# Kernel optimization log

Hardware: AMD Instinct MI355X
Metric: run time of the kernel (lower is better)

## Reference

```python
import jax, jax.numpy as jnp
import numpy as np

B, CIN, COUT, H, W, KH, KW, G = 16, 64, 128, 128, 128, 3, 3, 4


def setup_inputs() -> dict:
    key = jax.random.key(0)
    k1, k2, k3 = jax.random.split(key, 3)
    x = jax.random.normal(k1, (B, CIN, H, W), dtype=jnp.float32)
    spline_weights = jax.random.normal(k2, (COUT, CIN, KH, KW, G), dtype=jnp.float32)
    basis_weights = jax.random.normal(k3, (COUT, CIN, KH, KW), dtype=jnp.float32)
    return {"x": x, "spline_weights": spline_weights, "basis_weights": basis_weights}


def _conv_same(inp, w):
    # NCHW x OIHW -> NCHW, stride 1, SAME padding (pad = k//2, matches torch F.pad)
    return jax.lax.conv_general_dilated(
        inp, w, window_strides=(1, 1),
        padding=[(KH // 2, KH // 2), (KW // 2, KW // 2)],
        dimension_numbers=("NCHW", "OIHW", "NCHW"))


def reference(x, spline_weights, basis_weights):
    # spline branch: patch broadcast over grid then summed == conv with grid-summed kernel
    w_spline = spline_weights.sum(axis=-1)  # (COUT, CIN, KH, KW)
    # basis branch: silu applied to (zero-)padded patches; silu(0)=0 so equals conv(silu(x))
    return _conv_same(x, w_spline) + _conv_same(jax.nn.silu(x), basis_weights)
```

## Files before the change

kernel.cpp:

```cpp
#include <hip/hip_runtime.h>
#include <math.h>

#define B_    16
#define CIN   64
#define COUT  128
#define H_    128
#define W_    128
#define CI2   128
#define KTOT  1152

typedef __bf16 bf16x8 __attribute__((ext_vector_type(8)));
typedef float  f32x4  __attribute__((ext_vector_type(4)));

#define XT_BYTES  ((size_t)B_ * H_ * W_ * CI2 * 2)
#define WC_BYTES  ((size_t)COUT * KTOT * 2)
#define Z_OFF     (XT_BYTES + WC_BYTES)
#define WS_NEED   (Z_OFF + 4096)

__global__ __launch_bounds__(256) void w_prep(const float* __restrict__ sw,
                                              const float* __restrict__ bw,
                                              __bf16* __restrict__ wc,
                                              float* __restrict__ zp) {
    const int i = blockIdx.x * 256 + threadIdx.x;
    if (blockIdx.x == 0) zp[threadIdx.x] = 0.f;
    if (i >= COUT * KTOT) return;
    const int co = i / KTOT, k = i - co * KTOT;
    const int tap = k >> 7, ci2 = k & 127;
    float v;
    if (ci2 < CIN) {
        const float* p = sw + ((size_t)(co * CIN + ci2) * 9 + tap) * 4;
        v = p[0] + p[1] + p[2] + p[3];
    } else {
        v = bw[(size_t)(co * CIN + (ci2 - CIN)) * 9 + tap];
    }
    const int f = co >> 4, l15 = co & 15;
    const int kk = ci2 >> 6, j = (ci2 >> 5) & 1;
    const int lq = (ci2 >> 3) & 3, e = ci2 & 7;
    const int c = kk * 9 + tap;
    const size_t off = ((size_t)(c * 16 + f * 2 + j)) * 512 + (lq * 16 + l15) * 8 + e;
    wc[off] = (__bf16)v;
}

__global__ __launch_bounds__(256) void xt_prep(const float* __restrict__ x,
                                               __bf16* __restrict__ xt) {
    __shared__ __align__(16) __bf16 tile[64][136];
    const int t  = threadIdx.x;
    const int w0 = blockIdx.x * 64;
    const int h  = blockIdx.y;
    const int b  = blockIdx.z;
    const float* xb = x + ((size_t)(b * CIN) * H_ + h) * W_ + w0;
#pragma unroll
    for (int rep = 0; rep < 16; ++rep) {
        const int idx = rep * 256 + t;
        const int ci = idx >> 6, w = idx & 63;
        const float v = xb[(size_t)ci * H_ * W_ + w];
        tile[w][ci]       = (__bf16)v;
        tile[w][CIN + ci] = (__bf16)(v / (1.f + __expf(-v)));
    }
    __syncthreads();
    __bf16* ob = xt + (((size_t)b * H_ + h) * W_ + w0) * CI2;
#pragma unroll
    for (int rep = 0; rep < 4; ++rep) {
        const int idx = rep * 256 + t;
        const int w = idx >> 4, sl = idx & 15;
        *(bf16x8*)(ob + (size_t)w * CI2 + sl * 8) = *(const bf16x8*)(&tile[w][sl * 8]);
    }
}

__global__ __launch_bounds__(256, 2) void kan_mfma(const __bf16* __restrict__ xt,
                                                   const __bf16* __restrict__ wc,
                                                   const float* __restrict__ zp,
                                                   float* __restrict__ out) {
    __shared__ __align__(16) char bh[2720 * 16];
    __shared__ __align__(16) char asA[1024 * 16];
    __shared__ __align__(16) char asB[1024 * 16];
    const int t    = threadIdx.x;
    const int lane = t & 63, wn = t >> 6;
    const int l15 = lane & 15, lq = lane >> 4;

    const int orig = blockIdx.x;
    const int wid  = (orig & 7) * 128 + (orig >> 3);
    const int b  = wid >> 6;
    const int hy = (wid >> 2) & 15, wx = wid & 3;
    const int w0 = wx * 32, h0 = hy * 8;

    const size_t xbase = (size_t)b * (H_ * W_ * CI2);

#define STAGEB_(kk)                                                             \
    _Pragma("unroll")                                                           \
    for (int i = 0; i < 11; ++i) {                                              \
        const int s = i * 256 + t;                                              \
        if (s < 2720) {                                                         \
            const int cell = s >> 3, q = s & 7;                                 \
            const int ih = cell / 34, iw = cell - ih * 34;                      \
            const int gh = h0 + ih - 1, gw = w0 + iw - 1;                       \
            const int chunk = q ^ (cell & 7);                                   \
            const void* src;                                                    \
            if (gh >= 0 && gh < H_ && gw >= 0 && gw < W_)                       \
                src = (const void*)(xt + xbase +                                \
                      ((size_t)(gh * W_ + gw)) * CI2 + (kk) * 64 + chunk * 8);  \
            else                                                                \
                src = (const void*)zp;                                          \
            __builtin_amdgcn_global_load_lds(                                   \
                (const __attribute__((address_space(1))) unsigned int*)src,     \
                (__attribute__((address_space(3))) unsigned int*)(bh + s * 16), \
                16, 0, 0);                                                      \
        }                                                                       \
    }

#define STAGEC_(buf, c)                                                         \
    _Pragma("unroll")                                                           \
    for (int i = 0; i < 4; ++i) {                                               \
        const int s = i * 256 + t;                                              \
        __builtin_amdgcn_global_load_lds(                                       \
            (const __attribute__((address_space(1))) unsigned int*)              \
                (wc + (size_t)(c) * 8192 + s * 8),                              \
            (__attribute__((address_space(3))) unsigned int*)((buf) + s * 16),  \
            16, 0, 0);                                                          \
    }

#define COMPUTE_(buf, tp)                                                       \
    {                                                                           \
        const int kh_ = ((tp) * 11) >> 5;                                       \
        const int kw_ = (tp) - kh_ * 3;                                         \
        _Pragma("unroll")                                                       \
        for (int j = 0; j < 2; ++j) {                                           \
            bf16x8 af[8], bf[4];                                                \
            _Pragma("unroll")                                                   \
            for (int m = 0; m < 8; ++m)                                         \
                af[m] = *(const bf16x8*)((buf) + (m * 2 + j) * 1024 +           \
                                         lane * 16);                            \
            _Pragma("unroll")                                                   \
            for (int n = 0; n < 4; ++n) {                                       \
                const int cell = (wn * 2 + (n >> 1) + kh_) * 34 +               \
                                 (n & 1) * 16 + l15 + kw_;                      \
                const int swz  = (j * 4 + lq) ^ (cell & 7);                     \
                bf[n] = *(const bf16x8*)(bh + cell * 128 + swz * 16);           \
            }                                                                   \
            __builtin_amdgcn_s_setprio(1);                                      \
            _Pragma("unroll")                                                   \
            for (int m = 0; m < 8; ++m)                                         \
                _Pragma("unroll")                                               \
                for (int n = 0; n < 4; ++n)                                     \
                    acc[m][n] = __builtin_amdgcn_mfma_f32_16x16x32_bf16(        \
                        af[m], bf[n], acc[m][n], 0, 0, 0);                      \
            __builtin_amdgcn_s_setprio(0);                                      \
        }                                                                       \
    }

    f32x4 acc[8][4] = {};

    STAGEB_(0);
    STAGEC_(asA, 0);
    __syncthreads();

#pragma unroll 1
    for (int kk = 0; kk < 2; ++kk) {
        if (kk) {
            STAGEB_(1);
            __syncthreads();
        }
#pragma unroll 1
        for (int tap = 0; tap < 9; ++tap) {
            const int c = kk * 9 + tap;
            if (c < 17) STAGEC_((c & 1) ? asA : asB, c + 1);
            COMPUTE_((c & 1) ? asB : asA, tap);
            __syncthreads();
        }
    }

    float* ob = out + (size_t)b * COUT * H_ * W_;
#pragma unroll
    for (int m = 0; m < 8; ++m) {
        const int co = m * 16 + lq * 4;
#pragma unroll
        for (int n = 0; n < 4; ++n) {
            const int oh = h0 + wn * 2 + (n >> 1);
            const int ow = w0 + (n & 1) * 16 + l15;
            float* p = ob + ((size_t)co * H_ + oh) * W_ + ow;
#pragma unroll
            for (int r = 0; r < 4; ++r)
                p[(size_t)r * H_ * W_] = acc[m][n][r];
        }
    }
#undef STAGEB_
#undef STAGEC_
#undef COMPUTE_
}

#define TS   16
#define COB  8
#define TIN  18
__global__ __launch_bounds__(256) void spline_sum_kernel(const float* __restrict__ sw,
                                                         float* __restrict__ wsum) {
    int i = blockIdx.x * 256 + threadIdx.x;
    if (i < COUT * CIN * 9) {
        const float4 v = *reinterpret_cast<const float4*>(sw + (size_t)i * 4);
        wsum[i] = v.x + v.y + v.z + v.w;
    }
}
__global__ __launch_bounds__(256) void kan_conv(const float* __restrict__ x,
                                                const float* __restrict__ wsp,
                                                const float* __restrict__ wb,
                                                float* __restrict__ out) {
    __shared__ float xsm[TIN][20];
    __shared__ float ssm[TIN][20];
    const int t = threadIdx.x, tx = t & 15, ty = t >> 4;
    const int w0 = (blockIdx.x & 7) * TS, h0 = (blockIdx.x >> 3) * TS;
    const int co0 = blockIdx.y * COB, b = blockIdx.z;
    float acc[COB];
#pragma unroll
    for (int i = 0; i < COB; ++i) acc[i] = 0.f;
    const float* xb = x + (size_t)b * CIN * H_ * W_;
    for (int ci = 0; ci < CIN; ++ci) {
        __syncthreads();
        const float* xc = xb + (size_t)ci * H_ * W_;
        for (int p = t; p < TIN * TIN; p += 256) {
            int r = p / TIN, c = p - r * TIN;
            int ih = h0 + r - 1, iw = w0 + c - 1;
            float v = 0.f;
            if (ih >= 0 && ih < H_ && iw >= 0 && iw < W_) v = xc[ih * W_ + iw];
            xsm[r][c] = v;
            ssm[r][c] = v / (1.f + expf(-v));
        }
        __syncthreads();
        float xv[9], sv[9];
#pragma unroll
        for (int kh = 0; kh < 3; ++kh)
#pragma unroll
            for (int kw = 0; kw < 3; ++kw) {
                xv[kh * 3 + kw] = xsm[ty + kh][tx + kw];
                sv[kh * 3 + kw] = ssm[ty + kh][tx + kw];
            }
#pragma unroll
        for (int co = 0; co < COB; ++co) {
            const float* w1 = wsp + ((size_t)(co0 + co) * CIN + ci) * 9;
            const float* w2 = wb  + ((size_t)(co0 + co) * CIN + ci) * 9;
#pragma unroll
            for (int k = 0; k < 9; ++k)
                acc[co] += xv[k] * w1[k] + sv[k] * w2[k];
        }
    }
    const int oh = h0 + ty, ow = w0 + tx;
#pragma unroll
    for (int co = 0; co < COB; ++co)
        out[(((size_t)b * COUT + (co0 + co)) * H_ + oh) * W_ + ow] = acc[co];
}

extern "C" void kernel_launch(void* const* d_in, const int* in_sizes, int n_in,
                              void* d_out, int out_size, void* d_ws, size_t ws_size,
                              hipStream_t stream) {
    const float* x  = (const float*)d_in[0];
    const float* sw = (const float*)d_in[1];
    const float* bw = (const float*)d_in[2];
    float* out = (float*)d_out;

    if (ws_size >= WS_NEED) {
        __bf16* xt = (__bf16*)d_ws;
        __bf16* wc = (__bf16*)((char*)d_ws + XT_BYTES);
        float*  zp = (float*)((char*)d_ws + Z_OFF);
        w_prep<<<(COUT * KTOT + 255) / 256, 256, 0, stream>>>(sw, bw, wc, zp);
        xt_prep<<<dim3(2, H_, B_), 256, 0, stream>>>(x, xt);
        kan_mfma<<<dim3(1024), 256, 0, stream>>>(xt, wc, zp, out);
    } else {
        float* wsum = (float*)d_ws;
        spline_sum_kernel<<<(COUT * CIN * 9 + 255) / 256, 256, 0, stream>>>(sw, wsum);
        kan_conv<<<dim3(64, COUT / COB, B_), 256, 0, stream>>>(x, wsum, bw, out);
    }
}
```

Baseline: 100.2 us.

## Fuse input bf16/SiLU transpose into MFMA conv kernel, drop xt_prep pass

Removes the separate xt_prep kernel, which wrote a bf16 NHWC copy of x and silu(x) to workspace. The MFMA kernel now loads the fp32 NCHW input halo directly into shared scratch (reusing the weight buffer) in four channel passes. It converts to bf16 there, applying SiLU for the second K half, and writes the swizzled tile layout in place. This saves a full read and write of the intermediate tensor. The cost is extra synchronisation, SiLU being recomputed across overlapping halos, and less overlap between staging and compute.

Result: no change. 101.7 us (+1.4%).

```diff
diff --git a/kernel.cpp b/kernel.cpp
--- a/kernel.cpp
+++ b/kernel.cpp
@@ -12,17 +12,13 @@
 typedef __bf16 bf16x8 __attribute__((ext_vector_type(8)));
 typedef float  f32x4  __attribute__((ext_vector_type(4)));
 
-#define XT_BYTES  ((size_t)B_ * H_ * W_ * CI2 * 2)
 #define WC_BYTES  ((size_t)COUT * KTOT * 2)
-#define Z_OFF     (XT_BYTES + WC_BYTES)
-#define WS_NEED   (Z_OFF + 4096)
+#define WS_NEED   (WC_BYTES + 4096)
 
 __global__ __launch_bounds__(256) void w_prep(const float* __restrict__ sw,
                                               const float* __restrict__ bw,
-                                              __bf16* __restrict__ wc,
-                                              float* __restrict__ zp) {
+                                              __bf16* __restrict__ wc) {
     const int i = blockIdx.x * 256 + threadIdx.x;
-    if (blockIdx.x == 0) zp[threadIdx.x] = 0.f;
     if (i >= COUT * KTOT) return;
     const int co = i / KTOT, k = i - co * KTOT;
     const int tap = k >> 7, ci2 = k & 127;
@@ -41,35 +37,8 @@
     wc[off] = (__bf16)v;
 }
 
-__global__ __launch_bounds__(256) void xt_prep(const float* __restrict__ x,
-                                               __bf16* __restrict__ xt) {
-    __shared__ __align__(16) __bf16 tile[64][136];
-    const int t  = threadIdx.x;
-    const int w0 = blockIdx.x * 64;
-    const int h  = blockIdx.y;
-    const int b  = blockIdx.z;
-    const float* xb = x + ((size_t)(b * CIN) * H_ + h) * W_ + w0;
-#pragma unroll
-    for (int rep = 0; rep < 16; ++rep) {
-        const int idx = rep * 256 + t;
-        const int ci = idx >> 6, w = idx & 63;
-        const float v = xb[(size_t)ci * H_ * W_ + w];
-        tile[w][ci]       = (__bf16)v;
-        tile[w][CIN + ci] = (__bf16)(v / (1.f + __expf(-v)));
-    }
-    __syncthreads();
-    __bf16* ob = xt + (((size_t)b * H_ + h) * W_ + w0) * CI2;
-#pragma unroll
-    for (int rep = 0; rep < 4; ++rep) {
-        const int idx = rep * 256 + t;
-        const int w = idx >> 4, sl = idx & 15;
-        *(bf16x8*)(ob + (size_t)w * CI2 + sl * 8) = *(const bf16x8*)(&tile[w][sl * 8]);
-    }
-}
-
-__global__ __launch_bounds__(256, 2) void kan_mfma(const __bf16* __restrict__ xt,
+__global__ __launch_bounds__(256, 2) void kan_mfma(const float* __restrict__ x,
                                                    const __bf16* __restrict__ wc,
-                                                   const float* __restrict__ zp,
                                                    float* __restrict__ out) {
     __shared__ __align__(16) char bh[2720 * 16];
     __shared__ __align__(16) char asA[1024 * 16];
@@ -84,28 +53,54 @@
     const int hy = (wid >> 2) & 15, wx = wid & 3;
     const int w0 = wx * 32, h0 = hy * 8;
 
-    const size_t xbase = (size_t)b * (H_ * W_ * CI2);
-
-#define STAGEB_(kk)                                                             \
-    _Pragma("unroll")                                                           \
-    for (int i = 0; i < 11; ++i) {                                              \
-        const int s = i * 256 + t;                                              \
-        if (s < 2720) {                                                         \
-            const int cell = s >> 3, q = s & 7;                                 \
-            const int ih = cell / 34, iw = cell - ih * 34;                      \
-            const int gh = h0 + ih - 1, gw = w0 + iw - 1;                       \
-            const int chunk = q ^ (cell & 7);                                   \
-            const void* src;                                                    \
-            if (gh >= 0 && gh < H_ && gw >= 0 && gw < W_)                       \
-                src = (const void*)(xt + xbase +                                \
-                      ((size_t)(gh * W_ + gw)) * CI2 + (kk) * 64 + chunk * 8);  \
-            else                                                                \
-                src = (const void*)zp;                                          \
-            __builtin_amdgcn_global_load_lds(                                   \
-                (const __attribute__((address_space(1))) unsigned int*)src,     \
-                (__attribute__((address_space(3))) unsigned int*)(bh + s * 16), \
-                16, 0, 0);                                                      \
+    char* scratch = asA;
+
+#define STAGE_BH(kkv)                                                           \
+    _Pragma("unroll 1")                                                         \
+    for (int p = 0; p < 4; ++p) {                                               \
+        _Pragma("unroll")                                                       \
+        for (int i = 0; i < 7; ++i) {                                           \
+            const int s = i * 256 + t;                                          \
+            if (s < 1600) {                                                     \
+                const int cil = s / 100, rem = s - cil * 100;                   \
+                const int ih = rem / 10, c4 = rem - ih * 10;                    \
+                int gh = h0 + ih - 1;                                           \
+                gh = gh < 0 ? 0 : (gh > 127 ? 127 : gh);                        \
+                int gw0 = w0 + c4 * 4 - 4;                                      \
+                gw0 = gw0 < 0 ? 0 : (gw0 > 124 ? 124 : gw0);                    \
+                const float* src = x +                                          \
+                    (((size_t)(b * CIN + p * 16 + cil) * H_ + gh) * W_ + gw0);  \
+                __builtin_amdgcn_global_load_lds(                               \
+                    (const __attribute__((address_space(1))) unsigned int*)src, \
+                    (__attribute__((address_space(3))) unsigned int*)            \
+                        (scratch + s * 16), 16, 0, 0);                          \
+            }                                                                   \
         }                                                                       \
+        __syncthreads();                       \
+        _Pragma("unroll")                                                       \
+        for (int i = 0; i < 3; ++i) {                                           \
+            const int w = i * 256 + t;                                          \
+            if (w < 680) {                                                      \
+                const int cell = w >> 1, qo = w & 1;                            \
+                const int o = p * 2 + qo;                                       \
+                const int ih = cell / 34, iw = cell - ih * 34;                  \
+                const int gh = h0 + ih - 1, gw = w0 + iw - 1;                   \
+                const bool valid = (gh >= 0 && gh < H_ && gw >= 0 && gw < W_);  \
+                bf16x8 vv;                                                      \
+                _Pragma("unroll")                                               \
+                for (int e = 0; e < 8; ++e) {                                   \
+                    float f = 0.f;                                              \
+                    if (valid) {                                                \
+                        f = *(const float*)(scratch +                           \
+                            (((qo * 8 + e) * 10 + ih) * 40 + iw + 3) * 4);      \
+                        if (kkv) f = f / (1.f + __expf(-f));                    \
+                    }                                                           \
+                    vv[e] = (__bf16)f;                                          \
+                }                                                               \
+                *(bf16x8*)(bh + cell * 128 + (o ^ (cell & 7)) * 16) = vv;       \
+            }                                                                   \
+        }                                                                       \
+        __syncthreads();        \
     }
 
 #define STAGEC_(buf, c)                                                         \
@@ -150,23 +145,26 @@
 
     f32x4 acc[8][4] = {};
 
-    STAGEB_(0);
+    STAGE_BH(0)
     STAGEC_(asA, 0);
     __syncthreads();
-
 #pragma unroll 1
-    for (int kk = 0; kk < 2; ++kk) {
-        if (kk) {
-            STAGEB_(1);
-            __syncthreads();
-        }
+    for (int tap = 0; tap < 9; ++tap) {
+        const int c = tap;
+        if (c < 8) STAGEC_((c & 1) ? asA : asB, c + 1);
+        COMPUTE_((c & 1) ? asB : asA, tap);
+        __syncthreads();
+    }
+
+    STAGE_BH(1)
+    STAGEC_(asB, 9);
+    __syncthreads();
 #pragma unroll 1
-        for (int tap = 0; tap < 9; ++tap) {
-            const int c = kk * 9 + tap;
-            if (c < 17) STAGEC_((c & 1) ? asA : asB, c + 1);
-            COMPUTE_((c & 1) ? asB : asA, tap);
-            __syncthreads();
-        }
+    for (int tap = 0; tap < 9; ++tap) {
+        const int c = 9 + tap;
+        if (c < 17) STAGEC_((c & 1) ? asA : asB, c + 1);
+        COMPUTE_((c & 1) ? asB : asA, tap);
+        __syncthreads();
     }
 
     float* ob = out + (size_t)b * COUT * H_ * W_;
@@ -183,7 +181,7 @@
                 p[(size_t)r * H_ * W_] = acc[m][n][r];
         }
     }
-#undef STAGEB_
+#undef STAGE_BH
 #undef STAGEC_
 #undef COMPUTE_
 }
@@ -256,12 +254,9 @@
     float* out = (float*)d_out;
 
     if (ws_size >= WS_NEED) {
-        __bf16* xt = (__bf16*)d_ws;
-        __bf16* wc = (__bf16*)((char*)d_ws + XT_BYTES);
-        float*  zp = (float*)((char*)d_ws + Z_OFF);
-        w_prep<<<(COUT * KTOT + 255) / 256, 256, 0, stream>>>(sw, bw, wc, zp);
-        xt_prep<<<dim3(2, H_, B_), 256, 0, stream>>>(x, xt);
-        kan_mfma<<<dim3(1024), 256, 0, stream>>>(xt, wc, zp, out);
+        __bf16* wcp = (__bf16*)d_ws;
+        w_prep<<<(COUT * KTOT + 255) / 256, 256, 0, stream>>>(sw, bw, wcp);
+        kan_mfma<<<dim3(1024), 256, 0, stream>>>(x, wcp, out);
     } else {
         float* wsum = (float*)d_ws;
         spline_sum_kernel<<<(COUT * CIN * 9 + 255) / 256, 256, 0, stream>>>(sw, wsum);
```

## Store only bf16 x and compute SiLU in-LDS from the staged halo tile

Applied to the files above, without the earlier changes.

The prep kernel now writes only the bf16 copy of x (64 channels) instead of both x and silu(x) (128 channels), halving the intermediate buffer. The main MFMA kernel loads the halo tile once. After the spline-branch taps it applies SiLU in place in shared memory, then runs the basis-branch taps, so the second global halo load disappears. This removes intermediate write and read traffic at the cost of an extra in-LDS elementwise pass and barrier. SiLU is now computed from bf16-rounded x, which slightly changes rounding.

New measurement: 98.21 us. -2.0%, faster.

```diff
diff --git a/kernel.cpp b/kernel.cpp
--- a/kernel.cpp
+++ b/kernel.cpp
@@ -12,7 +12,7 @@
 typedef __bf16 bf16x8 __attribute__((ext_vector_type(8)));
 typedef float  f32x4  __attribute__((ext_vector_type(4)));
 
-#define XT_BYTES  ((size_t)B_ * H_ * W_ * CI2 * 2)
+#define XT_BYTES  ((size_t)B_ * H_ * W_ * CIN * 2)
 #define WC_BYTES  ((size_t)COUT * KTOT * 2)
 #define Z_OFF     (XT_BYTES + WC_BYTES)
 #define WS_NEED   (Z_OFF + 4096)
@@ -43,7 +43,7 @@
 
 __global__ __launch_bounds__(256) void xt_prep(const float* __restrict__ x,
                                                __bf16* __restrict__ xt) {
-    __shared__ __align__(16) __bf16 tile[64][136];
+    __shared__ __align__(16) __bf16 tile[64][72];
     const int t  = threadIdx.x;
     const int w0 = blockIdx.x * 64;
     const int h  = blockIdx.y;
@@ -53,17 +53,15 @@
     for (int rep = 0; rep < 16; ++rep) {
         const int idx = rep * 256 + t;
         const int ci = idx >> 6, w = idx & 63;
-        const float v = xb[(size_t)ci * H_ * W_ + w];
-        tile[w][ci]       = (__bf16)v;
-        tile[w][CIN + ci] = (__bf16)(v / (1.f + __expf(-v)));
+        tile[w][ci] = (__bf16)xb[(size_t)ci * H_ * W_ + w];
     }
     __syncthreads();
-    __bf16* ob = xt + (((size_t)b * H_ + h) * W_ + w0) * CI2;
-#pragma unroll
-    for (int rep = 0; rep < 4; ++rep) {
+    __bf16* ob = xt + (((size_t)b * H_ + h) * W_ + w0) * CIN;
+#pragma unroll
+    for (int rep = 0; rep < 2; ++rep) {
         const int idx = rep * 256 + t;
-        const int w = idx >> 4, sl = idx & 15;
-        *(bf16x8*)(ob + (size_t)w * CI2 + sl * 8) = *(const bf16x8*)(&tile[w][sl * 8]);
+        const int w = idx >> 3, sl = idx & 7;
+        *(bf16x8*)(ob + (size_t)w * CIN + sl * 8) = *(const bf16x8*)(&tile[w][sl * 8]);
     }
 }
 
@@ -84,9 +82,9 @@
     const int hy = (wid >> 2) & 15, wx = wid & 3;
     const int w0 = wx * 32, h0 = hy * 8;
 
-    const size_t xbase = (size_t)b * (H_ * W_ * CI2);
-
-#define STAGEB_(kk)                                                             \
+    const size_t xbase = (size_t)b * (H_ * W_ * CIN);
+
+#define STAGEB_()                                                               \
     _Pragma("unroll")                                                           \
     for (int i = 0; i < 11; ++i) {                                              \
         const int s = i * 256 + t;                                              \
@@ -98,7 +96,7 @@
             const void* src;                                                    \
             if (gh >= 0 && gh < H_ && gw >= 0 && gw < W_)                       \
                 src = (const void*)(xt + xbase +                                \
-                      ((size_t)(gh * W_ + gw)) * CI2 + (kk) * 64 + chunk * 8);  \
+                      ((size_t)(gh * W_ + gw)) * CIN + chunk * 8);              \
             else                                                                \
                 src = (const void*)zp;                                          \
             __builtin_amdgcn_global_load_lds(                                   \
@@ -150,23 +148,39 @@
 
     f32x4 acc[8][4] = {};
 
-    STAGEB_(0);
+    STAGEB_();
     STAGEC_(asA, 0);
     __syncthreads();
 
 #pragma unroll 1
-    for (int kk = 0; kk < 2; ++kk) {
-        if (kk) {
-            STAGEB_(1);
-            __syncthreads();
-        }
+    for (int tap = 0; tap < 9; ++tap) {
+        const int c = tap;
+        STAGEC_((c & 1) ? asA : asB, c + 1);
+        COMPUTE_((c & 1) ? asB : asA, tap);
+        __syncthreads();
+    }
+
+#pragma unroll
+    for (int i = 0; i < 11; ++i) {
+        const int s = i * 256 + t;
+        if (s < 2720) {
+            bf16x8 v = *(const bf16x8*)(bh + s * 16);
+#pragma unroll
+            for (int e = 0; e < 8; ++e) {
+                const float f = (float)v[e];
+                v[e] = (__bf16)(f / (1.f + __expf(-f)));
+            }
+            *(bf16x8*)(bh + s * 16) = v;
+        }
+    }
+    __syncthreads();
+
 #pragma unroll 1
-        for (int tap = 0; tap < 9; ++tap) {
-            const int c = kk * 9 + tap;
-            if (c < 17) STAGEC_((c & 1) ? asA : asB, c + 1);
-            COMPUTE_((c & 1) ? asB : asA, tap);
-            __syncthreads();
-        }
+    for (int tap = 0; tap < 9; ++tap) {
+        const int c = 9 + tap;
+        if (c < 17) STAGEC_((c & 1) ? asA : asB, c + 1);
+        COMPUTE_((c & 1) ? asB : asA, tap);
+        __syncthreads();
     }
 
     float* ob = out + (size_t)b * COUT * H_ * W_;
@@ -257,11 +271,11 @@
 
     if (ws_size >= WS_NEED) {
         __bf16* xt = (__bf16*)d_ws;
-        __bf16* wc = (__bf16*)((char*)d_ws + XT_BYTES);
+        __bf16* wcp = (__bf16*)((char*)d_ws + XT_BYTES);
         float*  zp = (float*)((char*)d_ws + Z_OFF);
-        w_prep<<<(COUT * KTOT + 255) / 256, 256, 0, stream>>>(sw, bw, wc, zp);
+        w_prep<<<(COUT * KTOT + 255) / 256, 256, 0, stream>>>(sw, bw, wcp, zp);
         xt_prep<<<dim3(2, H_, B_), 256, 0, stream>>>(x, xt);
-        kan_mfma<<<dim3(1024), 256, 0, stream>>>(xt, wc, zp, out);
+        kan_mfma<<<dim3(1024), 256, 0, stream>>>(xt, wcp, zp, out);
     } else {
         float* wsum = (float*)d_ws;
         spline_sum_kernel<<<(COUT * CIN * 9 + 255) / 256, 256, 0, stream>>>(sw, wsum);
```
